# Optimization experiments

Hardware: AMD Instinct MI355X
Metric: run time of the kernel (lower is better)

## Reference

```python
import jax, jax.numpy as jnp
import numpy as np

NEG_SLOPE = 0.2   # PyG GATConv default negative_slope
BN_EPS = 1e-5
N_NODES = 50000
N_EDGES = 600000
N_GRAPHS = 64


def _gat_conv(x, W, att_src, att_dst, bias, src, dst, heads, out_ch, concat):
    """PyG GATConv (eval mode, self-loops already appended to src/dst).
    x: [N, in], W: [in, heads*out_ch], att_*: [heads, out_ch], bias: [heads*out_ch] or [out_ch].
    """
    n = x.shape[0]
    h = (x @ W).reshape(n, heads, out_ch)                  # [N, H, C]
    a_s = jnp.sum(h * att_src[None], axis=-1)              # [N, H]
    a_d = jnp.sum(h * att_dst[None], axis=-1)              # [N, H]
    logit = jax.nn.leaky_relu(a_s[src] + a_d[dst], NEG_SLOPE)  # [E, H]
    # segment softmax over destination node (every node has a self-loop -> no empty segment)
    m = jax.ops.segment_max(logit, dst, num_segments=n)
    p = jnp.exp(logit - m[dst])
    denom = jax.ops.segment_sum(p, dst, num_segments=n)
    alpha = p / (denom[dst] + 1e-16)                       # [E, H]
    out = jax.ops.segment_sum(h[src] * alpha[:, :, None], dst, num_segments=n)  # [N, H, C]
    out = out.reshape(n, heads * out_ch) if concat else out.mean(axis=1)
    return out + bias


def _bn(x, gamma, beta):
    mu = x.mean(axis=0)
    var = x.var(axis=0)
    return (x - mu) * jax.lax.rsqrt(var + BN_EPS) * gamma + beta


def setup_inputs() -> dict:
    key = jax.random.key(0)
    ks = jax.random.split(key, 20)
    hidden = 64
    d1_in, d1_out, h1 = 5, hidden // 2, 4          # 5 -> 32x4 = 128
    d2_in, d2_out, h2 = hidden * 2, hidden // 2, 4  # 128 -> 32x4 = 128
    d3_in, d3_out, h3 = hidden * 2, hidden, 1       # 128 -> 64

    def glorot(k, shape):
        fan = shape[0] + shape[-1]
        return jax.random.normal(k, shape, dtype=jnp.float32) * np.sqrt(2.0 / fan)

    inp = {
        "x": jax.random.normal(ks[0], (N_NODES, d1_in), dtype=jnp.float32),
        "edge_index": jax.random.randint(ks[1], (2, N_EDGES), 0, N_NODES),
        "batch": jnp.sort(jax.random.randint(ks[2], (N_NODES,), 0, N_GRAPHS)),
        # conv1
        "W1": glorot(ks[3], (d1_in, h1 * d1_out)),
        "a1_src": glorot(ks[4], (h1, d1_out)),
        "a1_dst": glorot(ks[5], (h1, d1_out)),
        "b1": jnp.zeros((h1 * d1_out,), dtype=jnp.float32),
        "g1": jnp.ones((h1 * d1_out,), dtype=jnp.float32),
        "be1": jnp.zeros((h1 * d1_out,), dtype=jnp.float32),
        # conv2
        "W2": glorot(ks[6], (d2_in, h2 * d2_out)),
        "a2_src": glorot(ks[7], (h2, d2_out)),
        "a2_dst": glorot(ks[8], (h2, d2_out)),
        "b2": jnp.zeros((h2 * d2_out,), dtype=jnp.float32),
        "g2": jnp.ones((h2 * d2_out,), dtype=jnp.float32),
        "be2": jnp.zeros((h2 * d2_out,), dtype=jnp.float32),
        # conv3 (single head, concat=False)
        "W3": glorot(ks[9], (d3_in, h3 * d3_out)),
        "a3_src": glorot(ks[10], (h3, d3_out)),
        "a3_dst": glorot(ks[11], (h3, d3_out)),
        "b3": jnp.zeros((d3_out,), dtype=jnp.float32),
    }
    return inp


def reference(x, edge_index, batch, W1, a1_src, a1_dst, b1, g1, be1,
              W2, a2_src, a2_dst, b2, g2, be2, W3, a3_src, a3_dst, b3):
    n = x.shape[0]
    loops = jnp.arange(n)
    src = jnp.concatenate([edge_index[0], loops])  # PyG add_self_loops=True
    dst = jnp.concatenate([edge_index[1], loops])

    h = jax.nn.elu(_bn(_gat_conv(x, W1, a1_src, a1_dst, b1, src, dst, 4, 32, True), g1, be1))
    h = jax.nn.elu(_bn(_gat_conv(h, W2, a2_src, a2_dst, b2, src, dst, 4, 32, True), g2, be2))
    h = jax.nn.elu(_gat_conv(h, W3, a3_src, a3_dst, b3, src, dst, 1, 64, False))

    counts = jax.ops.segment_sum(jnp.ones((n,), h.dtype), batch, num_segments=N_GRAPHS)
    mean_pool = jax.ops.segment_sum(h, batch, num_segments=N_GRAPHS) / jnp.maximum(counts, 1.0)[:, None]
    max_pool = jax.ops.segment_max(h, batch, num_segments=N_GRAPHS)
    max_pool = jnp.where(counts[:, None] > 0, max_pool, 0.0)
    return jnp.concatenate([mean_pool, max_pool], axis=1)  # [G, 128]
```

## Files before the change

kernel.cpp:

```cpp
#include <hip/hip_runtime.h>
#include <math.h>

#define NEG_SLOPE 0.2f
#define BN_EPS 1e-5f

typedef __attribute__((ext_vector_type(8))) short short8;
typedef __attribute__((ext_vector_type(4))) float f32x4;

__device__ __forceinline__ float lrelu_f(float x){ return x > 0.f ? x : NEG_SLOPE * x; }
__device__ __forceinline__ float elu_f(float x){ return x > 0.f ? x : __expf(x) - 1.f; }

__device__ __forceinline__ unsigned short f2bf(float f){
    unsigned u = __float_as_uint(f);
    return (unsigned short)((u + 0x7fffu + ((u >> 16) & 1u)) >> 16);
}
__device__ __forceinline__ float bf_lo(unsigned v){ return __uint_as_float(v << 16); }
__device__ __forceinline__ float bf_hi(unsigned v){ return __uint_as_float(v & 0xffff0000u); }
__device__ __forceinline__ float bf2f(unsigned short b){ return __uint_as_float((unsigned)b << 16); }

__device__ __forceinline__ unsigned enc_f(float x){
    unsigned b = __float_as_uint(x);
    return (b & 0x80000000u) ? ~b : (b | 0x80000000u);
}
__device__ __forceinline__ float dec_f(unsigned u){
    return __uint_as_float((u & 0x80000000u) ? (u & 0x7FFFFFFFu) : ~u);
}

__global__ void k_count(const int* __restrict__ ei, int E0, int N, int* __restrict__ counts){
    int i = blockIdx.x * blockDim.x + threadIdx.x;
    int tot = E0 + N;
    if (i >= tot) return;
    int dst = (i < E0) ? ei[E0 + i] : (i - E0);
    atomicAdd(&counts[dst], 1);
}

__global__ void k_scan_part(const int* __restrict__ counts, int n, int* __restrict__ part){
    __shared__ int sh[256];
    int tid = threadIdx.x;
    int i = blockIdx.x * 256 + tid;
    int v = (i < n) ? counts[i] : 0;
    sh[tid] = v;
    __syncthreads();
    for (int o = 128; o > 0; o >>= 1){
        if (tid < o) sh[tid] += sh[tid + o];
        __syncthreads();
    }
    if (tid == 0) part[blockIdx.x] = sh[0];
}

__global__ void k_scan_top(int* __restrict__ part, int P, int n, int* __restrict__ row_ptr){
    __shared__ int sh[256];
    int tid = threadIdx.x;
    int v = (tid < P) ? part[tid] : 0;
    sh[tid] = v;
    __syncthreads();
    for (int o = 1; o < 256; o <<= 1){
        int t = (tid >= o) ? sh[tid - o] : 0;
        __syncthreads();
        sh[tid] += t;
        __syncthreads();
    }
    if (tid < P) part[tid] = sh[tid] - v;
    if (tid == 0) row_ptr[n] = sh[255];
}

__global__ void k_scan_write(const int* __restrict__ counts, const int* __restrict__ part,
                             int n, int* __restrict__ row_ptr){
    __shared__ int sh[256];
    int tid = threadIdx.x;
    int i = blockIdx.x * 256 + tid;
    int v = (i < n) ? counts[i] : 0;
    sh[tid] = v;
    __syncthreads();
    for (int o = 1; o < 256; o <<= 1){
        int t = (tid >= o) ? sh[tid - o] : 0;
        __syncthreads();
        sh[tid] += t;
        __syncthreads();
    }
    if (i < n) row_ptr[i] = part[blockIdx.x] + sh[tid] - v;
}

__global__ void k_scatter(const int* __restrict__ ei, int E0, int N,
                          const int* __restrict__ row_ptr, int* __restrict__ cursor,
                          int* __restrict__ csr_src){
    int i = blockIdx.x * blockDim.x + threadIdx.x;
    int tot = E0 + N;
    if (i >= tot) return;
    int src, dst;
    if (i < E0){ src = ei[i]; dst = ei[E0 + i]; } else { src = dst = i - E0; }
    int pos = atomicAdd(&cursor[dst], 1);
    csr_src[row_ptr[dst] + pos] = src;
}

__global__ void k_graph_ptr(const int* __restrict__ batch, int N, int G, int* __restrict__ gp){
    int i = blockIdx.x * blockDim.x + threadIdx.x;
    if (i >= N) return;
    int b = batch[i];
    if (i == 0){ for (int g = 0; g <= b; ++g) gp[g] = 0; }
    else { int pb = batch[i - 1]; for (int g = pb + 1; g <= b; ++g) gp[g] = i; }
    if (i == N - 1){ for (int g = b + 1; g <= G; ++g) gp[g] = N; }
}

__global__ void k_wprep(const float* __restrict__ W, int OUT, unsigned short* __restrict__ Wt){
    int i = blockIdx.x * 256 + threadIdx.x;
    if (i >= 128 * OUT) return;
    int k = i / OUT, c = i % OUT;
    Wt[c * 128 + k] = f2bf(W[i]);
}

__global__ void k_gemm1(const float* __restrict__ X, const float* __restrict__ W,
                        const float* __restrict__ atts, const float* __restrict__ attd,
                        unsigned short* __restrict__ h, float* __restrict__ as_,
                        float* __restrict__ ad_, int N){
    __shared__ float Wl[5 * 128];
    int tid = threadIdx.x;
    for (int i = tid; i < 5 * 128; i += 256) Wl[i] = W[i];
    __syncthreads();
    int c = tid & 127, local = tid >> 7;
    float as_c = atts[c], ad_c = attd[c];
    for (long node = (long)blockIdx.x * 2 + local; node < N; node += (long)gridDim.x * 2){
        float x0 = X[node * 5 + 0], x1 = X[node * 5 + 1], x2 = X[node * 5 + 2],
              x3 = X[node * 5 + 3], x4 = X[node * 5 + 4];
        float acc = x0 * Wl[c] + x1 * Wl[128 + c] + x2 * Wl[256 + c] +
                    x3 * Wl[384 + c] + x4 * Wl[512 + c];
        float vs = acc * as_c, vd = acc * ad_c;
#pragma unroll
        for (int m = 1; m < 32; m <<= 1){ vs += __shfl_xor(vs, m); vd += __shfl_xor(vd, m); }
        h[node * 128 + c] = f2bf(acc);
        if ((c & 31) == 0){ as_[node * 4 + (c >> 5)] = vs; ad_[node * 4 + (c >> 5)] = vd; }
    }
}

template<int OUT, int H, bool BN>
__launch_bounds__(256)
__global__ void k_gemm_mfma(const float* __restrict__ X, const unsigned short* __restrict__ Wt,
                            const float* __restrict__ atts, const float* __restrict__ attd,
                            const float* __restrict__ coefs, const float* __restrict__ coefb,
                            unsigned short* __restrict__ h, float* __restrict__ as_,
                            float* __restrict__ ad_, int N){
    constexpr int TM  = 64;
    constexpr int NCT = OUT / 16;
    constexpr int CPH = NCT / H;
    __shared__ unsigned short Xl[TM * 128];
    __shared__ unsigned short Wl[OUT * 128];
    int tid = threadIdx.x;
    long base = (long)blockIdx.x * TM;

    for (int i = tid; i < OUT * 16; i += 256){
        int r = i >> 4, g = i & 15;
        uint4 v = *(const uint4*)&Wt[r * 128 + g * 8];
        int gs = g ^ (r & 7);
        *(uint4*)&Wl[r * 128 + gs * 8] = v;
    }
    for (int i = tid; i < TM * 16; i += 256){
        int r = i >> 4, g = i & 15;
        long node = base + r;
        uint4 o;
        if (node < N){
            const float* xp = &X[node * 128 + g * 8];
            float f[8];
            *(float4*)&f[0] = *(const float4*)xp;
            *(float4*)&f[4] = *(const float4*)(xp + 4);
#pragma unroll
            for (int j = 0; j < 8; ++j){
                float v = f[j];
                if (BN) v = elu_f(fmaf(v, coefs[g * 8 + j], coefb[g * 8 + j]));
                f[j] = v;
            }
            o.x = (unsigned)f2bf(f[0]) | ((unsigned)f2bf(f[1]) << 16);
            o.y = (unsigned)f2bf(f[2]) | ((unsigned)f2bf(f[3]) << 16);
            o.z = (unsigned)f2bf(f[4]) | ((unsigned)f2bf(f[5]) << 16);
            o.w = (unsigned)f2bf(f[6]) | ((unsigned)f2bf(f[7]) << 16);
        } else {
            o.x = o.y = o.z = o.w = 0u;
        }
        int gs = g ^ (r & 7);
        *(uint4*)&Xl[r * 128 + gs * 8] = o;
    }
    __syncthreads();

    int wid = tid >> 6;
    int lane = tid & 63;
    int lr = lane & 15, lk = lane >> 4;

    short8 afrag[4];
    int arow = wid * 16 + lr;
#pragma unroll
    for (int ks = 0; ks < 4; ++ks){
        int g = ks * 4 + lk;
        int gs = g ^ (arow & 7);
        afrag[ks] = *(const short8*)&Xl[arow * 128 + gs * 8];
    }
    f32x4 acc[NCT];
#pragma unroll
    for (int ct = 0; ct < NCT; ++ct) acc[ct] = (f32x4){0.f, 0.f, 0.f, 0.f};
#pragma unroll
    for (int ct = 0; ct < NCT; ++ct){
        int brow = ct * 16 + lr;
#pragma unroll
        for (int ks = 0; ks < 4; ++ks){
            int g = ks * 4 + lk;
            int gs = g ^ (brow & 7);
            short8 bfrag = *(const short8*)&Wl[brow * 128 + gs * 8];
            acc[ct] = __builtin_amdgcn_mfma_f32_16x16x32_bf16(afrag[ks], bfrag, acc[ct], 0, 0, 0);
        }
    }
    float ps[H][4], pd[H][4];
#pragma unroll
    for (int hh = 0; hh < H; ++hh)
#pragma unroll
        for (int j = 0; j < 4; ++j){ ps[hh][j] = 0.f; pd[hh][j] = 0.f; }
#pragma unroll
    for (int ct = 0; ct < NCT; ++ct){
        int col = ct * 16 + lr;
        int hh = ct / CPH;
        float asv = atts[col], adv = attd[col];
#pragma unroll
        for (int j = 0; j < 4; ++j){
            float v = acc[ct][j];
            long node = base + wid * 16 + lk * 4 + j;
            if (node < N) h[node * OUT + col] = f2bf(v);
            ps[hh][j] += v * asv;
            pd[hh][j] += v * adv;
        }
    }
#pragma unroll
    for (int m = 1; m < 16; m <<= 1){
#pragma unroll
        for (int hh = 0; hh < H; ++hh)
#pragma unroll
            for (int j = 0; j < 4; ++j){
                ps[hh][j] += __shfl_xor(ps[hh][j], m);
                pd[hh][j] += __shfl_xor(pd[hh][j], m);
            }
    }
    if (lr == 0){
#pragma unroll
        for (int j = 0; j < 4; ++j){
            long node = base + wid * 16 + lk * 4 + j;
            if (node < N){
#pragma unroll
                for (int hh = 0; hh < H; ++hh){
                    as_[node * H + hh] = ps[hh][j];
                    ad_[node * H + hh] = pd[hh][j];
                }
            }
        }
    }
}

template<int C, int H, int ACT>
__global__ void k_agg(const unsigned short* __restrict__ h, const float* __restrict__ as_,
                      const float* __restrict__ ad_, const int* __restrict__ row_ptr,
                      const int* __restrict__ csr_src, const float* __restrict__ bias,
                      float* __restrict__ out, int N){
    constexpr int CPL = C / 64;
    constexpr int GROUP = C / H;
    int n = blockIdx.x;
    if (n >= N) return;
    int lane = threadIdx.x;
    int hh = (CPL * lane) / GROUP;
    float ad = ad_[n * H + hh];
    int beg = row_ptr[n], end = row_ptr[n + 1];
    float accx = 0.f, accy = 0.f, dn = 0.f;
    const unsigned* h32 = (const unsigned*)h;
    int e = beg;
    for (; e + 2 <= end; e += 2){
        int s0 = csr_src[e], s1 = csr_src[e + 1];
        float a0 = as_[s0 * H + hh], a1 = as_[s1 * H + hh];
        unsigned v0, v1; unsigned short w0, w1;
        if (CPL == 2){ v0 = h32[(long)s0 * 64 + lane]; v1 = h32[(long)s1 * 64 + lane]; }
        else { w0 = h[(long)s0 * 64 + lane]; w1 = h[(long)s1 * 64 + lane]; }
        float p0 = __expf(lrelu_f(a0 + ad));
        float p1 = __expf(lrelu_f(a1 + ad));
        dn += p0 + p1;
        if (CPL == 2){
            accx += p0 * bf_lo(v0) + p1 * bf_lo(v1);
            accy += p0 * bf_hi(v0) + p1 * bf_hi(v1);
        } else {
            accx += p0 * bf2f(w0) + p1 * bf2f(w1);
        }
    }
    if (e < end){
        int s0 = csr_src[e];
        float p0 = __expf(lrelu_f(as_[s0 * H + hh] + ad));
        dn += p0;
        if (CPL == 2){
            unsigned v0 = h32[(long)s0 * 64 + lane];
            accx += p0 * bf_lo(v0); accy += p0 * bf_hi(v0);
        } else {
            accx += p0 * bf2f(h[(long)s0 * 64 + lane]);
        }
    }
    float inv = 1.f / dn;
    if (CPL == 2){
        float vx = accx * inv + bias[2 * lane];
        float vy = accy * inv + bias[2 * lane + 1];
        if (ACT == 1){ vx = elu_f(vx); vy = elu_f(vy); }
        float2 o; o.x = vx; o.y = vy;
        *(float2*)&out[(long)n * C + 2 * lane] = o;
    } else {
        float v = accx * inv + bias[lane];
        if (ACT == 1) v = elu_f(v);
        out[(long)n * C + lane] = v;
    }
}

__launch_bounds__(256)
__global__ void k_bn_part(const float* __restrict__ x, int N,
                          float* __restrict__ ps, float* __restrict__ pq){
    __shared__ float4 lsum[256], lsq[256];
    int tid = threadIdx.x;
    int cq = tid & 31;
    int rg = tid >> 5;
    int rpb = (N + gridDim.x - 1) / gridDim.x;
    int lo = blockIdx.x * rpb;
    int hi = lo + rpb; if (hi > N) hi = N;
    float4 s = {0.f, 0.f, 0.f, 0.f}, q = {0.f, 0.f, 0.f, 0.f};
    int r = lo + rg;
    for (; r + 24 < hi; r += 32){
        float4 v0 = *(const float4*)&x[(long)r * 128 + cq * 4];
        float4 v1 = *(const float4*)&x[(long)(r + 8) * 128 + cq * 4];
        float4 v2 = *(const float4*)&x[(long)(r + 16) * 128 + cq * 4];
        float4 v3 = *(const float4*)&x[(long)(r + 24) * 128 + cq * 4];
        s.x += v0.x + v1.x + v2.x + v3.x;
        s.y += v0.y + v1.y + v2.y + v3.y;
        s.z += v0.z + v1.z + v2.z + v3.z;
        s.w += v0.w + v1.w + v2.w + v3.w;
        q.x += v0.x * v0.x + v1.x * v1.x + v2.x * v2.x + v3.x * v3.x;
        q.y += v0.y * v0.y + v1.y * v1.y + v2.y * v2.y + v3.y * v3.y;
        q.z += v0.z * v0.z + v1.z * v1.z + v2.z * v2.z + v3.z * v3.z;
        q.w += v0.w * v0.w + v1.w * v1.w + v2.w * v2.w + v3.w * v3.w;
    }
    for (; r < hi; r += 8){
        float4 v = *(const float4*)&x[(long)r * 128 + cq * 4];
        s.x += v.x; s.y += v.y; s.z += v.z; s.w += v.w;
        q.x += v.x * v.x; q.y += v.y * v.y; q.z += v.z * v.z; q.w += v.w * v.w;
    }
    lsum[tid] = s; lsq[tid] = q;
    __syncthreads();
    for (int o = 4; o > 0; o >>= 1){
        if (rg < o){
            float4 s2 = lsum[tid + o * 32], q2 = lsq[tid + o * 32];
            s.x += s2.x; s.y += s2.y; s.z += s2.z; s.w += s2.w;
            q.x += q2.x; q.y += q2.y; q.z += q2.z; q.w += q2.w;
            lsum[tid] = s; lsq[tid] = q;
        }
        __syncthreads();
    }
    if (rg == 0){
        *(float4*)&ps[(long)blockIdx.x * 128 + cq * 4] = s;
        *(float4*)&pq[(long)blockIdx.x * 128 + cq * 4] = q;
    }
}

__launch_bounds__(1024)
__global__ void k_bn_fin(const float* __restrict__ ps, const float* __restrict__ pq, int PB,
                         const float* __restrict__ g, const float* __restrict__ be,
                         float invN, float* __restrict__ cs, float* __restrict__ cb){
    __shared__ float sh_s[1024], sh_q[1024];
    int tid = threadIdx.x;
    int c = tid & 127, sl = tid >> 7;
    float s = 0.f, q = 0.f;
    for (int b = sl; b < PB; b += 8){
        s += ps[(long)b * 128 + c];
        q += pq[(long)b * 128 + c];
    }
    sh_s[tid] = s; sh_q[tid] = q;
    __syncthreads();
    for (int o = 4; o > 0; o >>= 1){
        if (sl < o){
            s += sh_s[tid + o * 128]; q += sh_q[tid + o * 128];
            sh_s[tid] = s; sh_q[tid] = q;
        }
        __syncthreads();
    }
    if (sl == 0){
        float mu = s * invN;
        float var = q * invN - mu * mu;
        float sc = g[c] * rsqrtf(var + BN_EPS);
        cs[c] = sc;
        cb[c] = be[c] - mu * sc;
    }
}

__global__ void k_pool_part(const float* __restrict__ x, const int* __restrict__ gp,
                            float* __restrict__ psum, unsigned* __restrict__ pmax){
    constexpr int S = 16;
    __shared__ float ssum[256], smax[256];
    int g = blockIdx.y;
    int split = blockIdx.x;
    int tid = threadIdx.x;
    int c = tid & 63, sub = tid >> 6;
    int beg = gp[g], end = gp[g + 1];
    int len = end - beg;
    int chunk = (len + S - 1) / S;
    int lo = beg + split * chunk;
    int hi = lo + chunk; if (hi > end) hi = end;
    if (lo >= hi) return;
    float s = 0.f, mx = -1e30f;
    for (int i = lo + sub; i < hi; i += 4){
        float v = x[(long)i * 64 + c];
        s += v; mx = fmaxf(mx, v);
    }
    ssum[tid] = s; smax[tid] = mx;
    __syncthreads();
    if (tid < 64){
        for (int k = 1; k < 4; ++k){ s += ssum[tid + 64 * k]; mx = fmaxf(mx, smax[tid + 64 * k]); }
        atomicAdd(&psum[g * 64 + c], s);
        atomicMax(&pmax[g * 64 + c], enc_f(mx));
    }
}

__global__ void k_pool_fin(const float* __restrict__ psum, const unsigned* __restrict__ pmax,
                           const int* __restrict__ gp, float* __restrict__ out){
    int g = blockIdx.x;
    int c = threadIdx.x;
    int cnt = gp[g + 1] - gp[g];
    float mean = (cnt > 0) ? psum[g * 64 + c] / (float)cnt : 0.f;
    float mx   = (cnt > 0) ? dec_f(pmax[g * 64 + c]) : 0.f;
    out[g * 128 + c]      = mean;
    out[g * 128 + 64 + c] = mx;
}

extern "C" void kernel_launch(void* const* d_in, const int* in_sizes, int n_in,
                              void* d_out, int out_size, void* d_ws, size_t ws_size,
                              hipStream_t stream){
    const float* x   = (const float*)d_in[0];
    const int*   ei  = (const int*)d_in[1];
    const int*   bat = (const int*)d_in[2];
    const float* W1  = (const float*)d_in[3];
    const float* a1s = (const float*)d_in[4];
    const float* a1d = (const float*)d_in[5];
    const float* b1  = (const float*)d_in[6];
    const float* g1  = (const float*)d_in[7];
    const float* be1 = (const float*)d_in[8];
    const float* W2  = (const float*)d_in[9];
    const float* a2s = (const float*)d_in[10];
    const float* a2d = (const float*)d_in[11];
    const float* b2  = (const float*)d_in[12];
    const float* g2  = (const float*)d_in[13];
    const float* be2 = (const float*)d_in[14];
    const float* W3  = (const float*)d_in[15];
    const float* a3s = (const float*)d_in[16];
    const float* a3d = (const float*)d_in[17];
    const float* b3  = (const float*)d_in[18];
    float* out = (float*)d_out;

    int N  = in_sizes[2];
    int E0 = in_sizes[1] / 2;
    int E  = E0 + N;
    const int G = 64;
    int P  = (N + 255) / 256;
    const int PB = 512;

    char* ws = (char*)d_ws;
    size_t off = 0;
    auto alloc = [&](size_t bytes) -> char* {
        char* p = ws + off;
        off += (bytes + 255) & ~(size_t)255;
        return p;
    };
    int*      counts  = (int*)alloc((size_t)N * 4);
    int*      cursor  = (int*)alloc((size_t)N * 4);
    float*    psum    = (float*)alloc((size_t)G * 64 * 4);
    unsigned* pmax    = (unsigned*)alloc((size_t)G * 64 * 4);
    size_t zero_bytes = off;
    int*   part    = (int*)alloc(256 * 4);
    int*   row_ptr = (int*)alloc((size_t)(N + 1) * 4);
    int*   csr     = (int*)alloc((size_t)E * 4);
    int*   gp      = (int*)alloc((size_t)(G + 1) * 4);
    float* as_buf  = (float*)alloc((size_t)N * 4 * 4);
    float* ad_buf  = (float*)alloc((size_t)N * 4 * 4);
    float* coefs   = (float*)alloc(128 * 4);
    float* coefb   = (float*)alloc(128 * 4);
    float* bn_ps   = (float*)alloc((size_t)PB * 128 * 4);
    float* bn_pq   = (float*)alloc((size_t)PB * 128 * 4);
    unsigned short* wt2 = (unsigned short*)alloc(128 * 128 * 2);
    unsigned short* wt3 = (unsigned short*)alloc(64 * 128 * 2);
    unsigned short* hbuf = (unsigned short*)alloc((size_t)N * 128 * 2);
    float* xcur    = (float*)alloc((size_t)N * 128 * 4);

    hipMemsetAsync(ws, 0, zero_bytes, stream);
    k_wprep<<<64, 256, 0, stream>>>(W2, 128, wt2);
    k_wprep<<<32, 256, 0, stream>>>(W3, 64, wt3);
    k_count<<<(E + 255) / 256, 256, 0, stream>>>(ei, E0, N, counts);
    k_scan_part<<<P, 256, 0, stream>>>(counts, N, part);
    k_scan_top<<<1, 256, 0, stream>>>(part, P, N, row_ptr);
    k_scan_write<<<P, 256, 0, stream>>>(counts, part, N, row_ptr);
    k_scatter<<<(E + 255) / 256, 256, 0, stream>>>(ei, E0, N, row_ptr, cursor, csr);
    k_graph_ptr<<<(N + 255) / 256, 256, 0, stream>>>(bat, N, G, gp);

    k_gemm1<<<2048, 256, 0, stream>>>(x, W1, a1s, a1d, hbuf, as_buf, ad_buf, N);
    k_agg<128, 4, 0><<<N, 64, 0, stream>>>(hbuf, as_buf, ad_buf, row_ptr, csr, b1, xcur, N);
    k_bn_part<<<PB, 256, 0, stream>>>(xcur, N, bn_ps, bn_pq);
    k_bn_fin<<<1, 1024, 0, stream>>>(bn_ps, bn_pq, PB, g1, be1, 1.f / N, coefs, coefb);

    k_gemm_mfma<128, 4, true><<<(N + 63) / 64, 256, 0, stream>>>(
        xcur, wt2, a2s, a2d, coefs, coefb, hbuf, as_buf, ad_buf, N);
    k_agg<128, 4, 0><<<N, 64, 0, stream>>>(hbuf, as_buf, ad_buf, row_ptr, csr, b2, xcur, N);
    k_bn_part<<<PB, 256, 0, stream>>>(xcur, N, bn_ps, bn_pq);
    k_bn_fin<<<1, 1024, 0, stream>>>(bn_ps, bn_pq, PB, g2, be2, 1.f / N, coefs, coefb);

    k_gemm_mfma<64, 1, true><<<(N + 63) / 64, 256, 0, stream>>>(
        xcur, wt3, a3s, a3d, coefs, coefb, hbuf, as_buf, ad_buf, N);
    k_agg<64, 1, 1><<<N, 64, 0, stream>>>(hbuf, as_buf, ad_buf, row_ptr, csr, b3, xcur, N);

    {
        dim3 grid(16, G);
        k_pool_part<<<grid, 256, 0, stream>>>(xcur, gp, psum, pmax);
        k_pool_fin<<<G, 64, 0, stream>>>(psum, pmax, gp, out);
    }
}
```

Baseline: 284.1 us.

## Fuse layer-1 GEMM into aggregation and merge prep kernels

Layer 1 no longer materializes h or the per-node attention scores. k_agg1 recomputes the 5-wide projection from raw X on the fly for each gathered source node, using precomputed W1·att vectors for the logits. The count, graph-pointer and weight-transpose prep kernels are merged into one launch, and the scan drops its top-level kernel by having each block reduce the preceding partials. This cuts launches and the 128-wide bf16 h round trip, at the cost of recomputing the projection per edge and an O(P) redundant reduction per scan block. The softmax skips the max-subtraction, which relies on the logits staying small enough not to overflow.

Measured after the change: 284.1 us. No clear change (-0.0%).

```diff
diff --git a/kernel.cpp b/kernel.cpp
--- a/kernel.cpp
+++ b/kernel.cpp
@@ -26,12 +26,49 @@
     return __uint_as_float((u & 0x80000000u) ? (u & 0x7FFFFFFFu) : ~u);
 }
 
-__global__ void k_count(const int* __restrict__ ei, int E0, int N, int* __restrict__ counts){
-    int i = blockIdx.x * blockDim.x + threadIdx.x;
-    int tot = E0 + N;
-    if (i >= tot) return;
-    int dst = (i < E0) ? ei[E0 + i] : (i - E0);
-    atomicAdd(&counts[dst], 1);
+__global__ void k_prep(const int* __restrict__ ei, int E0, int N, int Bc, int Bg,
+                       const int* __restrict__ batch, int G,
+                       int* __restrict__ counts, int* __restrict__ gp,
+                       const float* __restrict__ W1, const float* __restrict__ a1s,
+                       const float* __restrict__ a1d,
+                       const float* __restrict__ W2, const float* __restrict__ W3,
+                       unsigned short* __restrict__ wt2, unsigned short* __restrict__ wt3,
+                       float* __restrict__ u_s, float* __restrict__ u_d){
+    int b = blockIdx.x, tid = threadIdx.x;
+    if (b < Bc){
+        int i = b * 256 + tid, tot = E0 + N;
+        if (i < tot){
+            int dst = (i < E0) ? ei[E0 + i] : (i - E0);
+            atomicAdd(&counts[dst], 1);
+        }
+    } else if (b < Bc + Bg){
+        int i = (b - Bc) * 256 + tid;
+        if (i < N){
+            int bb = batch[i];
+            if (i == 0){ for (int g = 0; g <= bb; ++g) gp[g] = 0; }
+            else { int pb = batch[i - 1]; for (int g = pb + 1; g <= bb; ++g) gp[g] = i; }
+            if (i == N - 1){ for (int g = bb + 1; g <= G; ++g) gp[g] = N; }
+        }
+    } else if (b < Bc + Bg + 96){
+        int i = (b - Bc - Bg) * 256 + tid;
+        if (i < 128 * 128){
+            int k = i / 128, c = i % 128;
+            wt2[c * 128 + k] = f2bf(W2[i]);
+        } else if (i < 128 * 128 + 128 * 64){
+            int j = i - 128 * 128;
+            int k = j / 64, c = j % 64;
+            wt3[c * 128 + k] = f2bf(W3[j]);
+        }
+    } else {
+        if (tid < 40){
+            int t2 = tid % 20;
+            int k = t2 / 4, hh = t2 % 4;
+            const float* att = (tid < 20) ? a1s : a1d;
+            float s = 0.f;
+            for (int j = 0; j < 32; ++j) s += W1[k * 128 + hh * 32 + j] * att[hh * 32 + j];
+            if (tid < 20) u_s[k * 4 + hh] = s; else u_d[k * 4 + hh] = s;
+        }
+    }
 }
 
 __global__ void k_scan_part(const int* __restrict__ counts, int n, int* __restrict__ part){
@@ -48,10 +85,23 @@
     if (tid == 0) part[blockIdx.x] = sh[0];
 }
 
-__global__ void k_scan_top(int* __restrict__ part, int P, int n, int* __restrict__ row_ptr){
-    __shared__ int sh[256];
-    int tid = threadIdx.x;
-    int v = (tid < P) ? part[tid] : 0;
+__global__ void k_scan_write(const int* __restrict__ counts, const int* __restrict__ part,
+                             int n, int* __restrict__ row_ptr){
+    __shared__ int sh[256], rsh[256];
+    __shared__ int offs;
+    int tid = threadIdx.x, bid = blockIdx.x;
+    int po = 0;
+    for (int j = tid; j < bid; j += 256) po += part[j];
+    rsh[tid] = po;
+    __syncthreads();
+    for (int o = 128; o > 0; o >>= 1){
+        if (tid < o) rsh[tid] += rsh[tid + o];
+        __syncthreads();
+    }
+    if (tid == 0) offs = rsh[0];
+    __syncthreads();
+    int i = bid * 256 + tid;
+    int v = (i < n) ? counts[i] : 0;
     sh[tid] = v;
     __syncthreads();
     for (int o = 1; o < 256; o <<= 1){
@@ -60,25 +110,8 @@
         sh[tid] += t;
         __syncthreads();
     }
-    if (tid < P) part[tid] = sh[tid] - v;
-    if (tid == 0) row_ptr[n] = sh[255];
-}
-
-__global__ void k_scan_write(const int* __restrict__ counts, const int* __restrict__ part,
-                             int n, int* __restrict__ row_ptr){
-    __shared__ int sh[256];
-    int tid = threadIdx.x;
-    int i = blockIdx.x * 256 + tid;
-    int v = (i < n) ? counts[i] : 0;
-    sh[tid] = v;
-    __syncthreads();
-    for (int o = 1; o < 256; o <<= 1){
-        int t = (tid >= o) ? sh[tid - o] : 0;
-        __syncthreads();
-        sh[tid] += t;
-        __syncthreads();
-    }
-    if (i < n) row_ptr[i] = part[blockIdx.x] + sh[tid] - v;
+    if (i < n) row_ptr[i] = offs + sh[tid] - v;
+    if (bid == gridDim.x - 1 && tid == 255) row_ptr[n] = offs + sh[255];
 }
 
 __global__ void k_scatter(const int* __restrict__ ei, int E0, int N,
@@ -93,43 +126,61 @@
     csr_src[row_ptr[dst] + pos] = src;
 }
 
-__global__ void k_graph_ptr(const int* __restrict__ batch, int N, int G, int* __restrict__ gp){
-    int i = blockIdx.x * blockDim.x + threadIdx.x;
-    if (i >= N) return;
-    int b = batch[i];
-    if (i == 0){ for (int g = 0; g <= b; ++g) gp[g] = 0; }
-    else { int pb = batch[i - 1]; for (int g = pb + 1; g <= b; ++g) gp[g] = i; }
-    if (i == N - 1){ for (int g = b + 1; g <= G; ++g) gp[g] = N; }
-}
-
-__global__ void k_wprep(const float* __restrict__ W, int OUT, unsigned short* __restrict__ Wt){
-    int i = blockIdx.x * 256 + threadIdx.x;
-    if (i >= 128 * OUT) return;
-    int k = i / OUT, c = i % OUT;
-    Wt[c * 128 + k] = f2bf(W[i]);
-}
-
-__global__ void k_gemm1(const float* __restrict__ X, const float* __restrict__ W,
-                        const float* __restrict__ atts, const float* __restrict__ attd,
-                        unsigned short* __restrict__ h, float* __restrict__ as_,
-                        float* __restrict__ ad_, int N){
-    __shared__ float Wl[5 * 128];
-    int tid = threadIdx.x;
-    for (int i = tid; i < 5 * 128; i += 256) Wl[i] = W[i];
-    __syncthreads();
-    int c = tid & 127, local = tid >> 7;
-    float as_c = atts[c], ad_c = attd[c];
-    for (long node = (long)blockIdx.x * 2 + local; node < N; node += (long)gridDim.x * 2){
-        float x0 = X[node * 5 + 0], x1 = X[node * 5 + 1], x2 = X[node * 5 + 2],
-              x3 = X[node * 5 + 3], x4 = X[node * 5 + 4];
-        float acc = x0 * Wl[c] + x1 * Wl[128 + c] + x2 * Wl[256 + c] +
-                    x3 * Wl[384 + c] + x4 * Wl[512 + c];
-        float vs = acc * as_c, vd = acc * ad_c;
-#pragma unroll
-        for (int m = 1; m < 32; m <<= 1){ vs += __shfl_xor(vs, m); vd += __shfl_xor(vd, m); }
-        h[node * 128 + c] = f2bf(acc);
-        if ((c & 31) == 0){ as_[node * 4 + (c >> 5)] = vs; ad_[node * 4 + (c >> 5)] = vd; }
-    }
+__launch_bounds__(512)
+__global__ void k_agg1(const float* __restrict__ X, const float* __restrict__ W1,
+                       const float* __restrict__ u_s, const float* __restrict__ u_d,
+                       const int* __restrict__ row_ptr, const int* __restrict__ csr_src,
+                       const float* __restrict__ bias, float* __restrict__ out, int N){
+    int wid = threadIdx.x >> 6, lane = threadIdx.x & 63;
+    long n = (long)blockIdx.x * 8 + wid;
+    if (n >= N) return;
+    int hh = lane >> 4;
+    int c0 = lane * 2;
+    float2 wv[5]; float us[5], ud[5];
+#pragma unroll
+    for (int k = 0; k < 5; ++k){
+        wv[k] = *(const float2*)&W1[k * 128 + c0];
+        us[k] = u_s[k * 4 + hh];
+        ud[k] = u_d[k * 4 + hh];
+    }
+    float xd[5];
+#pragma unroll
+    for (int k = 0; k < 5; ++k) xd[k] = X[n * 5 + k];
+    float ad = xd[0]*ud[0] + xd[1]*ud[1] + xd[2]*ud[2] + xd[3]*ud[3] + xd[4]*ud[4];
+    int beg = row_ptr[n], end = row_ptr[n + 1];
+    float accx = 0.f, accy = 0.f, dn = 0.f;
+    int e = beg;
+    for (; e + 2 <= end; e += 2){
+        int s0 = csr_src[e], s1 = csr_src[e + 1];
+        float a0[5], a1[5];
+#pragma unroll
+        for (int k = 0; k < 5; ++k){ a0[k] = X[(long)s0 * 5 + k]; a1[k] = X[(long)s1 * 5 + k]; }
+        float as0 = a0[0]*us[0] + a0[1]*us[1] + a0[2]*us[2] + a0[3]*us[3] + a0[4]*us[4];
+        float as1 = a1[0]*us[0] + a1[1]*us[1] + a1[2]*us[2] + a1[3]*us[3] + a1[4]*us[4];
+        float p0 = __expf(lrelu_f(as0 + ad));
+        float p1 = __expf(lrelu_f(as1 + ad));
+        float hx0 = a0[0]*wv[0].x + a0[1]*wv[1].x + a0[2]*wv[2].x + a0[3]*wv[3].x + a0[4]*wv[4].x;
+        float hy0 = a0[0]*wv[0].y + a0[1]*wv[1].y + a0[2]*wv[2].y + a0[3]*wv[3].y + a0[4]*wv[4].y;
+        float hx1 = a1[0]*wv[0].x + a1[1]*wv[1].x + a1[2]*wv[2].x + a1[3]*wv[3].x + a1[4]*wv[4].x;
+        float hy1 = a1[0]*wv[0].y + a1[1]*wv[1].y + a1[2]*wv[2].y + a1[3]*wv[3].y + a1[4]*wv[4].y;
+        dn += p0 + p1;
+        accx += p0 * hx0 + p1 * hx1;
+        accy += p0 * hy0 + p1 * hy1;
+    }
+    if (e < end){
+        int s0 = csr_src[e];
+        float a0[5];
+#pragma unroll
+        for (int k = 0; k < 5; ++k) a0[k] = X[(long)s0 * 5 + k];
+        float as0 = a0[0]*us[0] + a0[1]*us[1] + a0[2]*us[2] + a0[3]*us[3] + a0[4]*us[4];
+        float p0 = __expf(lrelu_f(as0 + ad));
+        float hx0 = a0[0]*wv[0].x + a0[1]*wv[1].x + a0[2]*wv[2].x + a0[3]*wv[3].x + a0[4]*wv[4].x;
+        float hy0 = a0[0]*wv[0].y + a0[1]*wv[1].y + a0[2]*wv[2].y + a0[3]*wv[3].y + a0[4]*wv[4].y;
+        dn += p0; accx += p0 * hx0; accy += p0 * hy0;
+    }
+    float inv = 1.f / dn;
+    float2 o; o.x = accx * inv + bias[c0]; o.y = accy * inv + bias[c0 + 1];
+    *(float2*)&out[n * 128 + c0] = o;
 }
 
 template<int OUT, int H, bool BN>
@@ -475,6 +526,8 @@
     float* ad_buf  = (float*)alloc((size_t)N * 4 * 4);
     float* coefs   = (float*)alloc(128 * 4);
     float* coefb   = (float*)alloc(128 * 4);
+    float* u_s     = (float*)alloc(20 * 4);
+    float* u_d     = (float*)alloc(20 * 4);
     float* bn_ps   = (float*)alloc((size_t)PB * 128 * 4);
     float* bn_pq   = (float*)alloc((size_t)PB * 128 * 4);
     unsigned short* wt2 = (unsigned short*)alloc(128 * 128 * 2);
@@ -483,17 +536,15 @@
     float* xcur    = (float*)alloc((size_t)N * 128 * 4);
 
     hipMemsetAsync(ws, 0, zero_bytes, stream);
-    k_wprep<<<64, 256, 0, stream>>>(W2, 128, wt2);
-    k_wprep<<<32, 256, 0, stream>>>(W3, 64, wt3);
-    k_count<<<(E + 255) / 256, 256, 0, stream>>>(ei, E0, N, counts);
+
+    int Bc = (E + 255) / 256, Bg = (N + 255) / 256;
+    k_prep<<<Bc + Bg + 96 + 1, 256, 0, stream>>>(ei, E0, N, Bc, Bg, bat, G, counts, gp,
+                                                 W1, a1s, a1d, W2, W3, wt2, wt3, u_s, u_d);
     k_scan_part<<<P, 256, 0, stream>>>(counts, N, part);
-    k_scan_top<<<1, 256, 0, stream>>>(part, P, N, row_ptr);
     k_scan_write<<<P, 256, 0, stream>>>(counts, part, N, row_ptr);
     k_scatter<<<(E + 255) / 256, 256, 0, stream>>>(ei, E0, N, row_ptr, cursor, csr);
-    k_graph_ptr<<<(N + 255) / 256, 256, 0, stream>>>(bat, N, G, gp);
-
-    k_gemm1<<<2048, 256, 0, stream>>>(x, W1, a1s, a1d, hbuf, as_buf, ad_buf, N);
-    k_agg<128, 4, 0><<<N, 64, 0, stream>>>(hbuf, as_buf, ad_buf, row_ptr, csr, b1, xcur, N);
+
+    k_agg1<<<(N + 7) / 8, 512, 0, stream>>>(x, W1, u_s, u_d, row_ptr, csr, b1, xcur, N);
     k_bn_part<<<PB, 256, 0, stream>>>(xcur, N, bn_ps, bn_pq);
     k_bn_fin<<<1, 1024, 0, stream>>>(bn_ps, bn_pq, PB, g1, be1, 1.f / N, coefs, coefb);
 
```
